# Kernel optimization log

Hardware: AMD Instinct MI355X
Metric: run time of the kernel (lower is better)

The kernel has to match this reference:

```python
import jax, jax.numpy as jnp
import numpy as np

B, LQ, LKV, D = 8, 2048, 2048, 1024

def setup_inputs() -> dict:
    key = jax.random.key(0)
    k1, k2, k3, k4, k5, k6, k7 = jax.random.split(key, 7)
    s = 1.0 / np.sqrt(D)
    return {
        "query": jax.random.normal(k1, (B, LQ, D), jnp.float32),
        "key": jax.random.normal(k2, (B, LKV, D), jnp.float32),
        "value": jax.random.normal(k3, (B, LKV, D), jnp.float32),
        "Wq": jax.random.uniform(k4, (D, D), jnp.float32, -s, s),
        "bq": jax.random.uniform(k5, (D,), jnp.float32, -s, s),
        "Wk": jax.random.uniform(k6, (D, D), jnp.float32, -s, s),
        "bk": jax.random.uniform(k7, (D,), jnp.float32, -s, s),
        "scale_factor": 32,
        "dropout_p": 0,
    }

def reference(query, key, value, Wq, bq, Wk, bk, scale_factor, dropout_p):
    # q/k linear projections (torch Linear: x @ W^T + b); v is used raw per the source
    q = jnp.einsum("bld,ed->ble", query, Wq) + bq
    k = jnp.einsum("bld,ed->ble", key, Wk) + bk
    scores = jnp.einsum("bqd,bkd->bqk", q, k) / jnp.float32(scale_factor)
    attn = jax.nn.softmax(scores, axis=-1)
    # dropout_p == 0 -> identity (deterministic baseline)
    return jnp.einsum("bqk,bkd->bqd", attn, value)
```

## Files before the change

kernel.cpp:

```cpp
#include <hip/hip_runtime.h>

typedef __bf16 bf16;
typedef __attribute__((ext_vector_type(4))) __bf16 bf16x4;
typedef __attribute__((ext_vector_type(8))) __bf16 bf16x8;
typedef __attribute__((ext_vector_type(4))) float f32x4;

__device__ __forceinline__ void gload_lds16(const void* g, void* l) {
  __builtin_amdgcn_global_load_lds(
      (const __attribute__((address_space(1))) unsigned int*)(unsigned long long)g,
      (__attribute__((address_space(3))) unsigned int*)(unsigned long long)l,
      16, 0, 0);
}

__global__ void cast_f32_bf16(const float* __restrict__ in, bf16* __restrict__ out, int n4) {
  int i = blockIdx.x * blockDim.x + threadIdx.x;
  if (i >= n4) return;
  float4 v = reinterpret_cast<const float4*>(in)[i];
  bf16x4 o;
  o[0] = (bf16)v.x; o[1] = (bf16)v.y; o[2] = (bf16)v.z; o[3] = (bf16)v.w;
  reinterpret_cast<bf16x4*>(out)[i] = o;
}

__global__ void transpose_cast(const float* __restrict__ V, bf16* __restrict__ VT,
                               int rows, int cols) {
  __shared__ bf16 tile[64][65];
  const int b = blockIdx.z;
  const float* Vb = V + (long)b * rows * cols;
  bf16* VTb = VT + (long)b * rows * cols;
  const int d0 = blockIdx.x * 64;
  const int k0 = blockIdx.y * 64;
  const int t = threadIdx.x;
  const int r = t >> 4;
  const int c4 = (t & 15) * 4;
#pragma unroll
  for (int p = 0; p < 4; ++p) {
    float4 v = *reinterpret_cast<const float4*>(&Vb[(long)(k0 + p * 16 + r) * cols + d0 + c4]);
    tile[p * 16 + r][c4 + 0] = (bf16)v.x;
    tile[p * 16 + r][c4 + 1] = (bf16)v.y;
    tile[p * 16 + r][c4 + 2] = (bf16)v.z;
    tile[p * 16 + r][c4 + 3] = (bf16)v.w;
  }
  __syncthreads();
#pragma unroll
  for (int p = 0; p < 4; ++p) {
    const int dd = p * 16 + r;
    bf16x4 o;
    o[0] = tile[c4 + 0][dd];
    o[1] = tile[c4 + 1][dd];
    o[2] = tile[c4 + 2][dd];
    o[3] = tile[c4 + 3][dd];
    *reinterpret_cast<bf16x4*>(&VTb[(long)(d0 + dd) * rows + k0 + c4]) = o;
  }
}

__global__ void softmax_rows(bf16* __restrict__ S) {
  const long row = blockIdx.x;
  bf16* p = S + row * 2048;
  const int t = threadIdx.x;
  const int wid = t >> 6;
  const int lane = t & 63;
  bf16x8 v = *reinterpret_cast<bf16x8*>(p + t * 8);
  float f[8];
  float m = -3.0e38f;
#pragma unroll
  for (int j = 0; j < 8; ++j) { f[j] = (float)v[j]; m = fmaxf(m, f[j]); }
#pragma unroll
  for (int off = 32; off >= 1; off >>= 1) m = fmaxf(m, __shfl_xor(m, off));
  __shared__ float redm[4], reds[4];
  if (lane == 0) redm[wid] = m;
  __syncthreads();
  m = fmaxf(fmaxf(redm[0], redm[1]), fmaxf(redm[2], redm[3]));
  float s = 0.f;
#pragma unroll
  for (int j = 0; j < 8; ++j) { f[j] = __expf(f[j] - m); s += f[j]; }
#pragma unroll
  for (int off = 32; off >= 1; off >>= 1) s += __shfl_xor(s, off);
  if (lane == 0) reds[wid] = s;
  __syncthreads();
  s = reds[0] + reds[1] + reds[2] + reds[3];
  const float inv = 1.0f / s;
  bf16x8 o;
#pragma unroll
  for (int j = 0; j < 8; ++j) o[j] = (bf16)(f[j] * inv);
  *reinterpret_cast<bf16x8*>(p + t * 8) = o;
}


#define STAGE(buf, ko)                          \
  {                                             \
    bf16* lA_ = ldsA + (buf) * 12288;           \
    bf16* lB_ = ldsB + (buf) * 12288;           \
    gload_lds16(gA + (ko), lA_);                \
    gload_lds16(gB + (ko), lB_);                \
    gload_lds16(gB + (ko) + rK128, lB_ + 4096); \
  }

#define LOADA(buf)                                                             \
  _Pragma("unroll") for (int m_ = 0; m_ < 4; ++m_)                             \
      a[m_] = *reinterpret_cast<const bf16x8*>(aB + (buf) * 12288 + m_ * 512);
#define LOADB(buf)                                                             \
  _Pragma("unroll") for (int n_ = 0; n_ < 4; ++n_)                             \
      b[n_] = *reinterpret_cast<const bf16x8*>(bB + (buf) * 12288 + n_ * 512);

#define MFMAP                                                                  \
  _Pragma("unroll") for (int m_ = 0; m_ < 4; ++m_)                             \
  _Pragma("unroll") for (int n_ = 0; n_ < 4; ++n_)                             \
      acc[m_][n_] = __builtin_amdgcn_mfma_f32_16x16x32_bf16(                   \
          a[m_], b[n_], acc[m_][n_], 0, 0, 0);

template <int MODE>
__global__ __launch_bounds__(512, 4)
void gemm_bt(const bf16* __restrict__ A, const bf16* __restrict__ Bm,
             const float* __restrict__ bias0, const float* __restrict__ bias1,
             void* __restrict__ Cvoid, const int* __restrict__ scale_ptr,
             int N, int K, long sA, long sB, long sC) {
  __shared__ bf16 lds[2][12288];
  const int t = threadIdx.x;
  const int lane = t & 63;
  const int wid = t >> 6;
  const int wm = wid >> 2;
  const int wn = wid & 3;

  const int gx = gridDim.x, gy = gridDim.y;
  const int nwg = gx * gy * gridDim.z;
  int id = blockIdx.x + gx * (blockIdx.y + gy * blockIdx.z);
  {
    const int cpx = nwg >> 3;
    id = (id & 7) * cpx + (id >> 3);
  }
  const int bx = id % gx;
  const int by = (id / gx) % gy;
  const int bz = id / (gx * gy);

  const bf16* Ab = A + (long)bz * sA;
  const bf16* Bb = Bm + (long)bz * sB;
  const int tile_m = by * 128;
  const int tile_n = bx * 256;

  const int srow = t >> 2;
  const int soff = (((t & 3) ^ ((t >> 3) & 3)) << 3);
  const bf16* gA = Ab + (long)(tile_m + srow) * K + soff;
  const bf16* gB = Bb + (long)(tile_n + srow) * K + soff;
  const long rK128 = (long)K << 7;
  bf16* const ldsA = &lds[0][0] + wid * 512;
  bf16* const ldsB = &lds[0][4096] + wid * 512;

  const int frow = lane & 15;
  const int pko = (((lane >> 4) ^ ((lane >> 1) & 3)) << 3);
  const bf16* aB = &lds[0][0] + (wm * 64 + frow) * 32 + pko;
  const bf16* bB = &lds[0][4096] + (wn * 64 + frow) * 32 + pko;

  bf16x8 a[4], b[4];
  f32x4 acc[4][4] = {};

  STAGE(0, 0)
  __syncthreads();

  const int NK = K >> 5;
  int c = 0;
  for (int kt = 0; kt < NK - 1; ++kt, c ^= 1) {
    STAGE(c ^ 1, (long)(kt + 1) << 5)
    LOADB(c)
    LOADA(c)
    MFMAP
    __syncthreads();
  }
  LOADB(c)
  LOADA(c)
  MFMAP

  float scl = 1.0f;
  if (MODE == 1) {
    const int iv = scale_ptr[0];
    const float fv = __int_as_float(iv);
    const float sv = (iv > 0 && iv < (1 << 20)) ? (float)iv : fv;
    scl = 1.0f / sv;
  }
  const int rb = tile_m + wm * 64 + ((lane >> 4) << 2);
  const int cb = tile_n + wn * 64 + (lane & 15);
  if (MODE == 2) {
    float* C = reinterpret_cast<float*>(Cvoid) + (long)bz * sC;
#pragma unroll
    for (int mf = 0; mf < 4; ++mf)
#pragma unroll
      for (int nf = 0; nf < 4; ++nf)
#pragma unroll
        for (int r = 0; r < 4; ++r)
          C[(long)(rb + mf * 16 + r) * N + (cb + nf * 16)] = acc[mf][nf][r];
  } else {
    bf16* C = reinterpret_cast<bf16*>(Cvoid) + (long)bz * sC;
    const float* bias = (MODE == 0) ? (bz ? bias1 : bias0) : nullptr;
#pragma unroll
    for (int nf = 0; nf < 4; ++nf) {
      const int col = cb + nf * 16;
      const float bv = (MODE == 0) ? bias[col] : 0.0f;
#pragma unroll
      for (int mf = 0; mf < 4; ++mf)
#pragma unroll
        for (int r = 0; r < 4; ++r)
          C[(long)(rb + mf * 16 + r) * N + col] = (bf16)(acc[mf][nf][r] * scl + bv);
    }
  }
}

extern "C" void kernel_launch(void* const* d_in, const int* in_sizes, int n_in,
                              void* d_out, int out_size, void* d_ws, size_t ws_size,
                              hipStream_t stream) {
  (void)in_sizes; (void)n_in; (void)out_size; (void)ws_size;
  const float* query = (const float*)d_in[0];
  const float* key   = (const float*)d_in[1];
  const float* value = (const float*)d_in[2];
  const float* Wq    = (const float*)d_in[3];
  const float* bq    = (const float*)d_in[4];
  const float* Wk    = (const float*)d_in[5];
  const float* bk    = (const float*)d_in[6];
  const int*   scale = (const int*)d_in[7];

  const int L = 2048, D = 1024;
  char* ws = (char*)d_ws;
  bf16* q_cast = (bf16*)ws;
  bf16* k_cast = q_cast + (long)16384 * 1024;
  bf16* S      = q_cast;
  bf16* Qp     = (bf16*)(ws + (size_t)67108864);
  bf16* Kp     = (bf16*)(ws + (size_t)100663296);
  bf16* VT     = (bf16*)(ws + (size_t)134217728);
  bf16* Wqb    = (bf16*)(ws + (size_t)167772160);
  bf16* Wkb    = (bf16*)(ws + (size_t)169869312);

  cast_f32_bf16<<<16384, 256, 0, stream>>>(query, q_cast, 4194304);
  cast_f32_bf16<<<16384, 256, 0, stream>>>(key,   k_cast, 4194304);
  cast_f32_bf16<<<1024,  256, 0, stream>>>(Wq, Wqb, 262144);
  cast_f32_bf16<<<1024,  256, 0, stream>>>(Wk, Wkb, 262144);
  transpose_cast<<<dim3(16, 32, 8), 256, 0, stream>>>(value, VT, 2048, 1024);

  gemm_bt<0><<<dim3(4, 128, 2), 512, 0, stream>>>(q_cast, Wqb, bq, bk, Qp, nullptr,
                                                  1024, 1024,
                                                  16777216L, 1048576L, 16777216L);
  gemm_bt<1><<<dim3(8, 16, 8), 512, 0, stream>>>(Qp, Kp, nullptr, nullptr, S, scale,
                                                 2048, 1024,
                                                 (long)L * D, (long)L * D, (long)L * L);
  softmax_rows<<<16384, 256, 0, stream>>>(S);
  gemm_bt<2><<<dim3(4, 16, 8), 512, 0, stream>>>(S, VT, nullptr, nullptr, d_out, nullptr,
                                                 1024, 2048,
                                                 (long)L * L, (long)D * L, (long)L * D);
}
```

Measured before the change: 298.2 us.

## Enlarge GEMM tiles to 256x256 with triple-buffered LDS and register double-buffering

The GEMM kernel now computes a 256x256 output tile per workgroup instead of 128x256, with each wave owning 8x4 MFMA fragments. Its LDS staging uses three buffers with vmcnt-based waits, and fragment loads are double-buffered in registers so the next k-step's LDS reads overlap the current MFMAs. The aim is more data reuse per byte loaded and hidden global/LDS latency. In exchange, register pressure rises (launch bounds drop to 2 waves/EU), grids shrink, and clamped redundant prefetches run at the tail.

```diff
diff --git a/kernel.cpp b/kernel.cpp
--- a/kernel.cpp
+++ b/kernel.cpp
@@ -86,35 +86,45 @@
 }
 
 
-#define STAGE(buf, ko)                          \
-  {                                             \
-    bf16* lA_ = ldsA + (buf) * 12288;           \
-    bf16* lB_ = ldsB + (buf) * 12288;           \
-    gload_lds16(gA + (ko), lA_);                \
-    gload_lds16(gB + (ko), lB_);                \
-    gload_lds16(gB + (ko) + rK128, lB_ + 4096); \
-  }
-
-#define LOADA(buf)                                                             \
-  _Pragma("unroll") for (int m_ = 0; m_ < 4; ++m_)                             \
-      a[m_] = *reinterpret_cast<const bf16x8*>(aB + (buf) * 12288 + m_ * 512);
-#define LOADB(buf)                                                             \
+#define BARRIER __builtin_amdgcn_s_barrier()
+#define SCHED0 __builtin_amdgcn_sched_barrier(0)
+#define VM4                                                \
+  do {                                                     \
+    asm volatile("s_waitcnt vmcnt(4)" ::: "memory");       \
+  } while (0)
+
+#define STAGE(buf, ko)                                     \
+  {                                                        \
+    bf16* l_ = ldsw + (buf) * 16384;                       \
+    const long ko_ = (ko);                                 \
+    gload_lds16(gA + ko_, l_);                             \
+    gload_lds16(gA + ko_ + rK128, l_ + 4096);              \
+    gload_lds16(gB + ko_, l_ + 8192);                      \
+    gload_lds16(gB + ko_ + rK128, l_ + 12288);             \
+  }
+
+#define LOADA(dst, buf)                                                        \
+  _Pragma("unroll") for (int m_ = 0; m_ < 8; ++m_)                             \
+      dst[m_] = *reinterpret_cast<const bf16x8*>(aBase + (buf) * 16384 + m_ * 512);
+#define LOADB(dst, buf)                                                        \
   _Pragma("unroll") for (int n_ = 0; n_ < 4; ++n_)                             \
-      b[n_] = *reinterpret_cast<const bf16x8*>(bB + (buf) * 12288 + n_ * 512);
-
-#define MFMAP                                                                  \
-  _Pragma("unroll") for (int m_ = 0; m_ < 4; ++m_)                             \
+      dst[n_] = *reinterpret_cast<const bf16x8*>(bBase + (buf) * 16384 + n_ * 512);
+
+#define MFMA32(a_, b_)                                                         \
+  _Pragma("unroll") for (int m_ = 0; m_ < 8; ++m_)                             \
   _Pragma("unroll") for (int n_ = 0; n_ < 4; ++n_)                             \
       acc[m_][n_] = __builtin_amdgcn_mfma_f32_16x16x32_bf16(                   \
-          a[m_], b[n_], acc[m_][n_], 0, 0, 0);
+          a_[m_], b_[n_], acc[m_][n_], 0, 0, 0);
+
+#define ROT3 { int tmp_ = c0; c0 = c1; c1 = c2; c2 = tmp_; }
 
 template <int MODE>
-__global__ __launch_bounds__(512, 4)
+__global__ __launch_bounds__(512, 2)
 void gemm_bt(const bf16* __restrict__ A, const bf16* __restrict__ Bm,
              const float* __restrict__ bias0, const float* __restrict__ bias1,
              void* __restrict__ Cvoid, const int* __restrict__ scale_ptr,
              int N, int K, long sA, long sB, long sC) {
-  __shared__ bf16 lds[2][12288];
+  __shared__ bf16 lds[3][512][32];
   const int t = threadIdx.x;
   const int lane = t & 63;
   const int wid = t >> 6;
@@ -134,7 +144,7 @@
 
   const bf16* Ab = A + (long)bz * sA;
   const bf16* Bb = Bm + (long)bz * sB;
-  const int tile_m = by * 128;
+  const int tile_m = by * 256;
   const int tile_n = bx * 256;
 
   const int srow = t >> 2;
@@ -142,32 +152,51 @@
   const bf16* gA = Ab + (long)(tile_m + srow) * K + soff;
   const bf16* gB = Bb + (long)(tile_n + srow) * K + soff;
   const long rK128 = (long)K << 7;
-  bf16* const ldsA = &lds[0][0] + wid * 512;
-  bf16* const ldsB = &lds[0][4096] + wid * 512;
+  bf16* const ldsw = &lds[0][0][0] + wid * 512;
 
   const int frow = lane & 15;
   const int pko = (((lane >> 4) ^ ((lane >> 1) & 3)) << 3);
-  const bf16* aB = &lds[0][0] + (wm * 64 + frow) * 32 + pko;
-  const bf16* bB = &lds[0][4096] + (wn * 64 + frow) * 32 + pko;
-
-  bf16x8 a[4], b[4];
-  f32x4 acc[4][4] = {};
+  const bf16* aBase = &lds[0][0][0] + (wm * 128 + frow) * 32 + pko;
+  const bf16* bBase = &lds[0][0][0] + (256 + wn * 64 + frow) * 32 + pko;
+
+  bf16x8 aX[8], bX[4], aY[8], bY[4];
+  f32x4 acc[8][4] = {};
+
+  const int NK = K >> 5;
+  int c0 = 0, c1 = 1, c2 = 2;
 
   STAGE(0, 0)
-  __syncthreads();
-
-  const int NK = K >> 5;
-  int c = 0;
-  for (int kt = 0; kt < NK - 1; ++kt, c ^= 1) {
-    STAGE(c ^ 1, (long)(kt + 1) << 5)
-    LOADB(c)
-    LOADA(c)
-    MFMAP
-    __syncthreads();
-  }
-  LOADB(c)
-  LOADA(c)
-  MFMAP
+  STAGE(1, 32)
+  VM4;
+  BARRIER;
+  SCHED0;
+  LOADA(aX, 0)
+  LOADB(bX, 0)
+
+  for (int kt = 0; kt < NK; kt += 2) {
+    {
+      const long tt = (kt + 2 < NK) ? (long)(kt + 2) : (long)(NK - 1);
+      STAGE(c2, tt << 5)
+    }
+    VM4;
+    BARRIER;
+    SCHED0;
+    LOADA(aY, c1)
+    LOADB(bY, c1)
+    MFMA32(aX, bX)
+    ROT3
+    {
+      const long tt = (kt + 3 < NK) ? (long)(kt + 3) : (long)(NK - 1);
+      STAGE(c2, tt << 5)
+    }
+    VM4;
+    BARRIER;
+    SCHED0;
+    LOADA(aX, c1)
+    LOADB(bX, c1)
+    MFMA32(aY, bY)
+    ROT3
+  }
 
   float scl = 1.0f;
   if (MODE == 1) {
@@ -176,12 +205,12 @@
     const float sv = (iv > 0 && iv < (1 << 20)) ? (float)iv : fv;
     scl = 1.0f / sv;
   }
-  const int rb = tile_m + wm * 64 + ((lane >> 4) << 2);
+  const int rb = tile_m + wm * 128 + ((lane >> 4) << 2);
   const int cb = tile_n + wn * 64 + (lane & 15);
   if (MODE == 2) {
     float* C = reinterpret_cast<float*>(Cvoid) + (long)bz * sC;
 #pragma unroll
-    for (int mf = 0; mf < 4; ++mf)
+    for (int mf = 0; mf < 8; ++mf)
 #pragma unroll
       for (int nf = 0; nf < 4; ++nf)
 #pragma unroll
@@ -195,7 +224,7 @@
       const int col = cb + nf * 16;
       const float bv = (MODE == 0) ? bias[col] : 0.0f;
 #pragma unroll
-      for (int mf = 0; mf < 4; ++mf)
+      for (int mf = 0; mf < 8; ++mf)
 #pragma unroll
         for (int r = 0; r < 4; ++r)
           C[(long)(rb + mf * 16 + r) * N + col] = (bf16)(acc[mf][nf][r] * scl + bv);
@@ -233,14 +262,14 @@
   cast_f32_bf16<<<1024,  256, 0, stream>>>(Wk, Wkb, 262144);
   transpose_cast<<<dim3(16, 32, 8), 256, 0, stream>>>(value, VT, 2048, 1024);
 
-  gemm_bt<0><<<dim3(4, 128, 2), 512, 0, stream>>>(q_cast, Wqb, bq, bk, Qp, nullptr,
-                                                  1024, 1024,
-                                                  16777216L, 1048576L, 16777216L);
-  gemm_bt<1><<<dim3(8, 16, 8), 512, 0, stream>>>(Qp, Kp, nullptr, nullptr, S, scale,
-                                                 2048, 1024,
-                                                 (long)L * D, (long)L * D, (long)L * L);
+  gemm_bt<0><<<dim3(4, 64, 2), 512, 0, stream>>>(q_cast, Wqb, bq, bk, Qp, nullptr,
+                                                 1024, 1024,
+                                                 16777216L, 1048576L, 16777216L);
+  gemm_bt<1><<<dim3(8, 8, 8), 512, 0, stream>>>(Qp, Kp, nullptr, nullptr, S, scale,
+                                                2048, 1024,
+                                                (long)L * D, (long)L * D, (long)L * L);
   softmax_rows<<<16384, 256, 0, stream>>>(S);
-  gemm_bt<2><<<dim3(4, 16, 8), 512, 0, stream>>>(S, VT, nullptr, nullptr, d_out, nullptr,
-                                                 1024, 2048,
-                                                 (long)L * L, (long)D * L, (long)L * D);
-}
+  gemm_bt<2><<<dim3(4, 8, 8), 512, 0, stream>>>(S, VT, nullptr, nullptr, d_out, nullptr,
+                                                1024, 2048,
+                                                (long)L * L, (long)D * L, (long)L * D);
+}
```

New measurement: 299.9 us. About the same (+0.6%).
